# Performance work log

Hardware: AMD Instinct MI355X
Metric: run time of the kernel (lower is better)

Reference implementation:

```python
import jax, jax.numpy as jnp
import numpy as np

N = 100000   # nodes
E = 1600000  # edges (avg degree 16)
D = 128      # input feature dim
DIMS = [D, 64, 32, 16, 4]
K = 3


def setup_inputs() -> dict:
    key = jax.random.key(0)
    ks = jax.random.split(key, 8)
    inp = {
        "x": jax.random.normal(ks[0], (N, D), jnp.float32),
        "edge_index": jax.random.randint(ks[1], (2, E), 0, N, dtype=jnp.int32).astype(jnp.int64),
        "edge_weight": jax.random.uniform(ks[2], (E,), jnp.float32),
    }
    for i in range(4):
        fin, fout = DIMS[i], DIMS[i + 1]
        inp[f"W{i+1}"] = jax.random.normal(ks[3 + i], (K, fin, fout), jnp.float32) / np.sqrt(fin)
        inp[f"b{i+1}"] = jnp.zeros((fout,), jnp.float32)
    return inp


def reference(x, edge_index, edge_weight, W1, b1, W2, b2, W3, b3, W4, b4):
    # ChebConv, K=3, normalization='sym', lambda_max=2 (PyG defaults).
    # Scaled Laplacian L~ = 2L/lambda_max - I = -D^{-1/2} A D^{-1/2}
    n = x.shape[0]
    src, dst = edge_index[0], edge_index[1]
    deg = jax.ops.segment_sum(edge_weight, src, num_segments=n)
    dinv = jnp.where(deg > 0, jax.lax.rsqrt(deg), 0.0)
    norm = dinv[src] * edge_weight * dinv[dst]  # [E]

    def Lmul(h):  # L~ @ h  == -A_norm @ h
        return -jax.ops.segment_sum(norm[:, None] * h[src], dst, num_segments=n)

    def cheb(h, W, b):
        # Tx_0 = h, Tx_1 = L~ h, Tx_2 = 2 L~ Tx_1 - Tx_0
        Tx0 = h
        Tx1 = Lmul(h)
        Tx2 = 2.0 * Lmul(Tx1) - Tx0
        return Tx0 @ W[0] + Tx1 @ W[1] + Tx2 @ W[2] + b

    # training=False -> dropout is identity
    h = jax.nn.relu(cheb(x, W1, b1))
    h = jax.nn.relu(cheb(h, W2, b2))
    h = jax.nn.relu(cheb(h, W3, b3))
    h = cheb(h, W4, b4)
    return jax.nn.log_softmax(h, axis=1)
```

## Files before the change

### kernel.cpp

```cpp
#include <hip/hip_runtime.h>
#include <math.h>

#define D_IN 128
typedef unsigned short ushort_t;
typedef __attribute__((ext_vector_type(8))) short short8;
typedef __attribute__((ext_vector_type(4))) float f32x4;

__device__ __forceinline__ float bf2f(ushort_t u) {
    union { unsigned i; float f; } x;
    x.i = ((unsigned)u) << 16;
    return x.f;
}
__device__ __forceinline__ ushort_t f2bf(float f) {
    unsigned i = __float_as_uint(f);
    unsigned r = (i + 0x7fffu + ((i >> 16) & 1u)) >> 16;
    return (ushort_t)r;
}

#define CH 256
#define CHS 8
#define CAP 6144
#define MAXCH 512
#define NBIN 256

__global__ __launch_bounds__(256) void bin2_kernel(const int* __restrict__ src,
                                                   const int* __restrict__ dst,
                                                   const float* __restrict__ w,
                                                   int* __restrict__ gcA, int* __restrict__ gcB,
                                                   int2* __restrict__ stA,
                                                   int2* __restrict__ stB, int E, int nch) {
    __shared__ int cntA[MAXCH], baseA[MAXCH], posA[MAXCH];
    __shared__ int cntB[MAXCH], baseB[MAXCH], posB[MAXCH];
    for (int i = threadIdx.x; i < nch; i += 256) {
        cntA[i] = 0; posA[i] = 0; cntB[i] = 0; posB[i] = 0;
    }
    __syncthreads();
    int per = (E + gridDim.x - 1) / gridDim.x;
    int e0 = blockIdx.x * per, e1 = min(E, e0 + per);
    for (int e = e0 + threadIdx.x; e < e1; e += 256) {
        atomicAdd(&cntA[dst[e] >> CHS], 1);
        atomicAdd(&cntB[src[e] >> CHS], 1);
    }
    __syncthreads();
    for (int i = threadIdx.x; i < nch; i += 256) {
        int c = cntA[i];
        baseA[i] = c ? atomicAdd(&gcA[i], c) : 0;
        c = cntB[i];
        baseB[i] = c ? atomicAdd(&gcB[i], c) : 0;
    }
    __syncthreads();
    for (int e = e0 + threadIdx.x; e < e1; e += 256) {
        int s = src[e], d = dst[e];
        int wb = __float_as_int(w[e]);
        int cA = d >> CHS;
        int pA = baseA[cA] + atomicAdd(&posA[cA], 1);
        if (pA < CAP) {
            int2 o;
            o.x = s | ((d & (CH - 1)) << 17);
            o.y = wb;
            stA[(size_t)cA * CAP + pA] = o;
        }
        int cB = s >> CHS;
        int pB = baseB[cB] + atomicAdd(&posB[cB], 1);
        if (pB < CAP) {
            int2 o;
            o.x = s & (CH - 1);
            o.y = wb;
            stB[(size_t)cB * CAP + pB] = o;
        }
    }
}

__global__ __launch_bounds__(256) void deg_chunk_kernel(const int* __restrict__ gcB,
                                                        const int2* __restrict__ stB,
                                                        float* __restrict__ deg, int n) {
    __shared__ float acc[CH];
    int c = blockIdx.x, kb = blockIdx.y, KB = gridDim.y;
    for (int i = threadIdx.x; i < CH; i += 256) acc[i] = 0.f;
    __syncthreads();
    int m = min(gcB[c], CAP);
    int per = (m + KB - 1) / KB;
    int i0 = kb * per, i1 = min(m, i0 + per);
    size_t base = (size_t)c * CAP;
    for (int i = i0 + threadIdx.x; i < i1; i += 256) {
        int2 v = stB[base + i];
        atomicAdd(&acc[v.x], __int_as_float(v.y));
    }
    __syncthreads();
    int nb = c * CH, lim = min(CH, n - nb);
    for (int i = threadIdx.x; i < lim; i += 256) {
        float v = acc[i];
        if (v != 0.f) atomicAdd(&deg[nb + i], v);
    }
}

__global__ void dinv_kernel(float* __restrict__ deg, int n) {
    int i = blockIdx.x * blockDim.x + threadIdx.x;
    if (i >= n) return;
    float d = deg[i];
    deg[i] = (d > 0.f) ? rsqrtf(d) : 0.f;
}

__global__ __launch_bounds__(512) void cbase_kernel(const int* __restrict__ gcA,
                                                    int* __restrict__ cbase,
                                                    int* __restrict__ rp, int nch, int n) {
    __shared__ int sd[MAXCH];
    int t = threadIdx.x;
    sd[t] = (t < nch) ? min(gcA[t], CAP) : 0;
    __syncthreads();
    for (int off = 1; off < MAXCH; off <<= 1) {
        int y = (t >= off) ? sd[t - off] : 0;
        __syncthreads();
        sd[t] += y;
        __syncthreads();
    }
    if (t < nch) cbase[t] = (t > 0) ? sd[t - 1] : 0;
    if (t == 0) rp[n] = sd[nch - 1];
}

__global__ __launch_bounds__(256) void csr_chunk_kernel(const int* __restrict__ gcA,
                                                        const int* __restrict__ cbase,
                                                        const int2* __restrict__ stA,
                                                        const float* __restrict__ dinv,
                                                        int* __restrict__ rp,
                                                        int2* __restrict__ cv, int n) {
    __shared__ int lcnt[CH];
    __shared__ int lrp[CH];
    __shared__ float ldinv[CH];
    __shared__ int sdata[256];
    int c = blockIdx.x;
    int nb = c * CH, lim = min(CH, n - nb);
    int m = min(gcA[c], CAP);
    size_t sb = (size_t)c * CAP;
    int t = threadIdx.x;
    if (t < CH) lcnt[t] = 0;
    if (t < lim) ldinv[t] = dinv[nb + t];
    __syncthreads();
    for (int i = t; i < m; i += 256) atomicAdd(&lcnt[stA[sb + i].x >> 17], 1);
    __syncthreads();
    int v = (t < CH) ? lcnt[t] : 0;
    sdata[t] = v;
    __syncthreads();
    for (int off = 1; off < 256; off <<= 1) {
        int y = (t >= off) ? sdata[t - off] : 0;
        __syncthreads();
        sdata[t] += y;
        __syncthreads();
    }
    if (t < CH) lrp[t] = sdata[t] - v;
    __syncthreads();
    int base = cbase[c];
    if (t < lim) rp[nb + t] = base + lrp[t];
    if (t < CH) lcnt[t] = 0;
    __syncthreads();
    for (int i = t; i < m; i += 256) {
        int2 sv = stA[sb + i];
        int sN = sv.x & 0x1FFFF;
        int dl = sv.x >> 17;
        float nv = dinv[sN] * __int_as_float(sv.y) * ldinv[dl];
        int o = base + lrp[dl] + atomicAdd(&lcnt[dl], 1);
        int2 oo;
        oo.x = sN;
        oo.y = __float_as_int(nv);
        cv[o] = oo;
    }
}

__global__ void wt_all_kernel(const float* __restrict__ W1, const float* __restrict__ W2,
                              const float* __restrict__ W3, ushort_t* __restrict__ Wt1,
                              ushort_t* __restrict__ Wt2, ushort_t* __restrict__ Wt3) {
    int i = blockIdx.x * blockDim.x + threadIdx.x;
    if (i < 24576) {
        int m = i / 8192, rem = i % 8192, f = rem / 64, g = rem % 64;
        Wt1[((size_t)(m * 64 + g)) * 128 + f] = f2bf(W1[i]);
    } else if (i < 24576 + 6144) {
        int j = i - 24576;
        int m = j / 2048, rem = j % 2048, f = rem / 32, g = rem % 32;
        Wt2[((size_t)(m * 32 + g)) * 64 + f] = f2bf(W2[j]);
    } else if (i < 24576 + 6144 + 1536) {
        int j = i - 24576 - 6144;
        int m = j / 512, rem = j % 512, f = rem / 16, g = rem % 16;
        Wt3[((size_t)(m * 16 + g)) * 32 + f] = f2bf(W3[j]);
    }
}

template <int F, int G, bool A_BF16>
__global__ __launch_bounds__(256) void gemm_mfma(const void* __restrict__ Hv,
                                                 const ushort_t* __restrict__ Wt,
                                                 ushort_t* __restrict__ YA16,
                                                 ushort_t* __restrict__ YB16,
                                                 ushort_t* __restrict__ C16, int n) {
    constexpr int CT = G / 16;
    const int tid = threadIdx.x;
    const int wave = tid >> 6;
    const int lane = tid & 63;
    const int l16 = lane & 15;
    const int lk8 = (lane >> 4) * 8;

    const int rowBase = blockIdx.x * 64 + wave * 16;
    int rA = rowBase + l16;
    if (rA >= n) rA = n - 1;

    f32x4 acc[3][CT];
#pragma unroll
    for (int m = 0; m < 3; ++m)
#pragma unroll
        for (int ct = 0; ct < CT; ++ct)
#pragma unroll
            for (int j = 0; j < 4; ++j) acc[m][ct][j] = 0.f;

#pragma unroll
    for (int ks = 0; ks < F; ks += 32) {
        short8 a;
        if constexpr (A_BF16) {
            a = *(const short8*)((const ushort_t*)Hv + (size_t)rA * F + ks + lk8);
        } else {
            const float* ap = (const float*)Hv + (size_t)rA * F + ks + lk8;
            float4 f0 = *(const float4*)ap;
            float4 f1 = *(const float4*)(ap + 4);
            a[0] = (short)f2bf(f0.x);
            a[1] = (short)f2bf(f0.y);
            a[2] = (short)f2bf(f0.z);
            a[3] = (short)f2bf(f0.w);
            a[4] = (short)f2bf(f1.x);
            a[5] = (short)f2bf(f1.y);
            a[6] = (short)f2bf(f1.z);
            a[7] = (short)f2bf(f1.w);
        }
#pragma unroll
        for (int m = 0; m < 3; ++m) {
#pragma unroll
            for (int ct = 0; ct < CT; ++ct) {
                short8 b = *(const short8*)(Wt + ((size_t)(m * G + ct * 16 + l16)) * F +
                                            ks + lk8);
                acc[m][ct] = __builtin_amdgcn_mfma_f32_16x16x32_bf16(a, b, acc[m][ct], 0, 0, 0);
            }
        }
    }

    const int r0 = rowBase + (lane >> 4) * 4;
#pragma unroll
    for (int ct = 0; ct < CT; ++ct) {
        const int col = ct * 16 + l16;
#pragma unroll
        for (int j = 0; j < 4; ++j) {
            int r = r0 + j;
            if (r < n) {
                size_t idx = (size_t)r * G + col;
                YA16[idx] = f2bf(acc[0][ct][j] - acc[2][ct][j]);
                YB16[idx] = f2bf(acc[1][ct][j]);
                C16[idx] = f2bf(acc[2][ct][j]);
            }
        }
    }
}

template <int G, int MODE>
__global__ __launch_bounds__(256) void spmm_bf16(const ushort_t* __restrict__ Hg,
                                                 const ushort_t* __restrict__ Yres,
                                                 const float* __restrict__ bias,
                                                 ushort_t* __restrict__ outS,
                                                 const int2* __restrict__ cv,
                                                 const int* __restrict__ rp, int n) {
    constexpr int TPR = G / 4;
    constexpr int RPB = 256 / TPR;
    int row = blockIdx.x * RPB + threadIdx.x / TPR;
    if (row >= n) return;
    int g = (threadIdx.x % TPR) * 4;
    float a0 = 0.f, a1 = 0.f, a2 = 0.f, a3 = 0.f;
    int e = rp[row], e1 = rp[row + 1];
    for (; e + 4 <= e1; e += 4) {
        int2 c0 = cv[e], c1 = cv[e + 1], c2 = cv[e + 2], c3 = cv[e + 3];
        ushort4 h0 = *(const ushort4*)(Hg + (size_t)c0.x * G + g);
        ushort4 h1 = *(const ushort4*)(Hg + (size_t)c1.x * G + g);
        ushort4 h2 = *(const ushort4*)(Hg + (size_t)c2.x * G + g);
        ushort4 h3 = *(const ushort4*)(Hg + (size_t)c3.x * G + g);
        float v0 = __int_as_float(c0.y), v1 = __int_as_float(c1.y);
        float v2 = __int_as_float(c2.y), v3 = __int_as_float(c3.y);
        a0 = fmaf(v0, bf2f(h0.x), a0); a1 = fmaf(v0, bf2f(h0.y), a1);
        a2 = fmaf(v0, bf2f(h0.z), a2); a3 = fmaf(v0, bf2f(h0.w), a3);
        a0 = fmaf(v1, bf2f(h1.x), a0); a1 = fmaf(v1, bf2f(h1.y), a1);
        a2 = fmaf(v1, bf2f(h1.z), a2); a3 = fmaf(v1, bf2f(h1.w), a3);
        a0 = fmaf(v2, bf2f(h2.x), a0); a1 = fmaf(v2, bf2f(h2.y), a1);
        a2 = fmaf(v2, bf2f(h2.z), a2); a3 = fmaf(v2, bf2f(h2.w), a3);
        a0 = fmaf(v3, bf2f(h3.x), a0); a1 = fmaf(v3, bf2f(h3.y), a1);
        a2 = fmaf(v3, bf2f(h3.z), a2); a3 = fmaf(v3, bf2f(h3.w), a3);
    }
    for (; e < e1; ++e) {
        int2 c = cv[e];
        float v = __int_as_float(c.y);
        ushort4 hv = *(const ushort4*)(Hg + (size_t)c.x * G + g);
        a0 = fmaf(v, bf2f(hv.x), a0);
        a1 = fmaf(v, bf2f(hv.y), a1);
        a2 = fmaf(v, bf2f(hv.z), a2);
        a3 = fmaf(v, bf2f(hv.w), a3);
    }
    size_t idx = (size_t)row * G + g;
    ushort4 yv = *(const ushort4*)(Yres + idx);
    ushort4 o;
    if (MODE == 1) {
        o.x = f2bf(bf2f(yv.x) - 2.f * a0);
        o.y = f2bf(bf2f(yv.y) - 2.f * a1);
        o.z = f2bf(bf2f(yv.z) - 2.f * a2);
        o.w = f2bf(bf2f(yv.w) - 2.f * a3);
    } else {
        float4 bv = *(const float4*)(bias + g);
        o.x = f2bf(fmaxf(bf2f(yv.x) - a0 + bv.x, 0.f));
        o.y = f2bf(fmaxf(bf2f(yv.y) - a1 + bv.y, 0.f));
        o.z = f2bf(fmaxf(bf2f(yv.z) - a2 + bv.z, 0.f));
        o.w = f2bf(fmaxf(bf2f(yv.w) - a3 + bv.w, 0.f));
    }
    *(ushort4*)(outS + idx) = o;
}


__global__ void gemm4(const ushort_t* __restrict__ H, const float* __restrict__ W,
                      float* __restrict__ YA, float* __restrict__ YB, float* __restrict__ C,
                      int n) {
    __shared__ float Ws[3 * 16 * 4];
    if (threadIdx.x < 192) Ws[threadIdx.x] = W[threadIdx.x];
    __syncthreads();
    int i = blockIdx.x * blockDim.x + threadIdx.x;
    if (i >= n) return;
    const ushort_t* h = H + (size_t)i * 16;
    float a[4], b[4], c[4];
#pragma unroll
    for (int g = 0; g < 4; ++g) a[g] = b[g] = c[g] = 0.f;
#pragma unroll
    for (int j = 0; j < 2; ++j) {
        short8 hv = *(const short8*)(h + j * 8);
#pragma unroll
        for (int k = 0; k < 8; ++k) {
            int f = j * 8 + k;
            float hf = bf2f((ushort_t)hv[k]);
#pragma unroll
            for (int g = 0; g < 4; ++g) {
                a[g] = fmaf(hf, Ws[f * 4 + g], a[g]);
                b[g] = fmaf(hf, Ws[64 + f * 4 + g], b[g]);
                c[g] = fmaf(hf, Ws[128 + f * 4 + g], c[g]);
            }
        }
    }
    float4 oa, ob, oc;
    oa.x = a[0] - c[0]; oa.y = a[1] - c[1]; oa.z = a[2] - c[2]; oa.w = a[3] - c[3];
    ob.x = b[0]; ob.y = b[1]; ob.z = b[2]; ob.w = b[3];
    oc.x = c[0]; oc.y = c[1]; oc.z = c[2]; oc.w = c[3];
    *(float4*)(YA + (size_t)i * 4) = oa;
    *(float4*)(YB + (size_t)i * 4) = ob;
    *(float4*)(C + (size_t)i * 4) = oc;
}

__global__ void spmm4(const float* __restrict__ C, const float* __restrict__ YB,
                      float* __restrict__ S, const int2* __restrict__ cv,
                      const int* __restrict__ rp, int n) {
    int row = blockIdx.x * blockDim.x + threadIdx.x;
    if (row >= n) return;
    float a0 = 0.f, a1 = 0.f, a2 = 0.f, a3 = 0.f;
    int e1 = rp[row + 1];
    for (int e = rp[row]; e < e1; ++e) {
        int2 c = cv[e];
        float v = __int_as_float(c.y);
        float4 cvv = *(const float4*)(C + (size_t)c.x * 4);
        a0 = fmaf(v, cvv.x, a0);
        a1 = fmaf(v, cvv.y, a1);
        a2 = fmaf(v, cvv.z, a2);
        a3 = fmaf(v, cvv.w, a3);
    }
    float4 yb = *(const float4*)(YB + (size_t)row * 4);
    float4 o;
    o.x = yb.x - 2.f * a0;
    o.y = yb.y - 2.f * a1;
    o.z = yb.z - 2.f * a2;
    o.w = yb.w - 2.f * a3;
    *(float4*)(S + (size_t)row * 4) = o;
}

__global__ void layer4_final(const float* __restrict__ S, const float* __restrict__ YA,
                             const float* __restrict__ b, float* __restrict__ out,
                             const int2* __restrict__ cv, const int* __restrict__ rp, int n) {
    int row = blockIdx.x * blockDim.x + threadIdx.x;
    if (row >= n) return;
    float a0 = 0.f, a1 = 0.f, a2 = 0.f, a3 = 0.f;
    int e1 = rp[row + 1];
    for (int e = rp[row]; e < e1; ++e) {
        int2 c = cv[e];
        float v = __int_as_float(c.y);
        float4 sv = *(const float4*)(S + (size_t)c.x * 4);
        a0 = fmaf(v, sv.x, a0);
        a1 = fmaf(v, sv.y, a1);
        a2 = fmaf(v, sv.z, a2);
        a3 = fmaf(v, sv.w, a3);
    }
    float4 ya = *(const float4*)(YA + (size_t)row * 4);
    float o0 = ya.x - a0 + b[0];
    float o1 = ya.y - a1 + b[1];
    float o2 = ya.z - a2 + b[2];
    float o3 = ya.w - a3 + b[3];
    float m = fmaxf(fmaxf(o0, o1), fmaxf(o2, o3));
    float s = expf(o0 - m) + expf(o1 - m) + expf(o2 - m) + expf(o3 - m);
    float ls = m + logf(s);
    float4 r;
    r.x = o0 - ls;
    r.y = o1 - ls;
    r.z = o2 - ls;
    r.w = o3 - ls;
    *(float4*)(out + (size_t)row * 4) = r;
}


static inline char* align_up(char* p, size_t a) {
    return (char*)(((uintptr_t)p + a - 1) & ~(uintptr_t)(a - 1));
}

extern "C" void kernel_launch(void* const* d_in, const int* in_sizes, int n_in,
                              void* d_out, int out_size, void* d_ws, size_t ws_size,
                              hipStream_t stream) {
    const float* x = (const float*)d_in[0];
    const int* ei = (const int*)d_in[1];
    const float* ew = (const float*)d_in[2];
    const float* W1 = (const float*)d_in[3];
    const float* b1 = (const float*)d_in[4];
    const float* W2 = (const float*)d_in[5];
    const float* b2 = (const float*)d_in[6];
    const float* W3 = (const float*)d_in[7];
    const float* b3 = (const float*)d_in[8];
    const float* W4 = (const float*)d_in[9];
    const float* b4 = (const float*)d_in[10];
    float* out = (float*)d_out;

    const int n = in_sizes[0] / D_IN;
    const int E = in_sizes[2];
    const int* src = ei;
    const int* dst = ei + E;
    const int nch = (n + CH - 1) / CH;

    char* p = (char*)d_ws;
    int2* cv = (int2*)p;          p += (size_t)E * 8;
    float* deg = (float*)p;       p += (size_t)n * 4;
    int* rp = (int*)p;            p = align_up(p + (size_t)(n + 1) * 4, 64);
    int* gcA = (int*)p;           p += MAXCH * 4;
    int* gcB = (int*)p;           p += MAXCH * 4;
    int* cbase = (int*)p;         p = align_up(p + MAXCH * 4, 64);
    ushort_t* Wt1 = (ushort_t*)p; p = align_up(p + (size_t)192 * 128 * 2, 64);
    ushort_t* Wt2 = (ushort_t*)p; p = align_up(p + (size_t)96 * 64 * 2, 64);
    ushort_t* Wt3 = (ushort_t*)p; p = align_up(p + (size_t)48 * 32 * 2, 64);
    char* big = p;
    ushort_t* YA16 = (ushort_t*)big;
    ushort_t* YB16 = (ushort_t*)(big + (size_t)n * 64 * 2);
    ushort_t* C16 = (ushort_t*)(big + (size_t)n * 64 * 2 * 2);
    ushort_t* S16 = (ushort_t*)(big + (size_t)n * 64 * 2 * 3);
    int2* stA = (int2*)big;
    int2* stB = (int2*)(big + (size_t)nch * CAP * 8);
    p = align_up(big + (size_t)n * 64 * 2 * 4, 64);
    ushort_t* H1 = (ushort_t*)p;  p = align_up(p + (size_t)n * 64 * 2, 64);
    ushort_t* H2 = (ushort_t*)p;  p = align_up(p + (size_t)n * 32 * 2, 64);
    ushort_t* H3 = (ushort_t*)p;  p = align_up(p + (size_t)n * 16 * 2, 64);
    float* YA4 = (float*)p;       p = align_up(p + (size_t)n * 4 * 4, 64);
    float* YB4 = (float*)p;       p = align_up(p + (size_t)n * 4 * 4, 64);
    float* C4 = (float*)p;        p = align_up(p + (size_t)n * 4 * 4, 64);
    float* S4 = (float*)p;        p = align_up(p + (size_t)n * 4 * 4, 64);

    const int TB = 256;
    int nb256 = (n + TB - 1) / TB;
    int gm = (n + 63) / 64;

    hipMemsetAsync(deg, 0, (size_t)n * 4, stream);
    hipMemsetAsync(gcA, 0, MAXCH * 4 * 2, stream);
    bin2_kernel<<<NBIN, 256, 0, stream>>>(src, dst, ew, gcA, gcB, stA, stB, E, nch);
    {
        dim3 dg(nch, 4);
        deg_chunk_kernel<<<dg, 256, 0, stream>>>(gcB, stB, deg, n);
    }
    dinv_kernel<<<nb256, TB, 0, stream>>>(deg, n);
    cbase_kernel<<<1, MAXCH, 0, stream>>>(gcA, cbase, rp, nch, n);
    csr_chunk_kernel<<<nch, 256, 0, stream>>>(gcA, cbase, stA, deg, rp, cv, n);

    wt_all_kernel<<<(24576 + 6144 + 1536 + 255) / 256, 256, 0, stream>>>(W1, W2, W3, Wt1,
                                                                         Wt2, Wt3);

    {
        constexpr int G = 64;
        gemm_mfma<128, G, false><<<gm, 256, 0, stream>>>(x, Wt1, YA16, YB16, C16, n);
        int sb = (n + (1024 / G) - 1) / (1024 / G);
        spmm_bf16<G, 1><<<sb, 256, 0, stream>>>(C16, YB16, nullptr, S16, cv, rp, n);
        spmm_bf16<G, 2><<<sb, 256, 0, stream>>>(S16, YA16, b1, H1, cv, rp, n);
    }
    {
        constexpr int G = 32;
        gemm_mfma<64, G, true><<<gm, 256, 0, stream>>>(H1, Wt2, YA16, YB16, C16, n);
        int sb = (n + (1024 / G) - 1) / (1024 / G);
        spmm_bf16<G, 1><<<sb, 256, 0, stream>>>(C16, YB16, nullptr, S16, cv, rp, n);
        spmm_bf16<G, 2><<<sb, 256, 0, stream>>>(S16, YA16, b2, H2, cv, rp, n);
    }
    {
        constexpr int G = 16;
        gemm_mfma<32, G, true><<<gm, 256, 0, stream>>>(H2, Wt3, YA16, YB16, C16, n);
        int sb = (n + (1024 / G) - 1) / (1024 / G);
        spmm_bf16<G, 1><<<sb, 256, 0, stream>>>(C16, YB16, nullptr, S16, cv, rp, n);
        spmm_bf16<G, 2><<<sb, 256, 0, stream>>>(S16, YA16, b3, H3, cv, rp, n);
    }
    {
        gemm4<<<nb256, 256, 0, stream>>>(H3, W4, YA4, YB4, C4, n);
        spmm4<<<nb256, 256, 0, stream>>>(C4, YB4, S4, cv, rp, n);
        layer4_final<<<nb256, 256, 0, stream>>>(S4, YA4, b4, out, cv, rp, n);
    }
}
```

Measured before the change: 399.7 us.

## Widen binning blocks, double GEMM row tile per wave, unroll SpMM gather by 8

Three separate changes. The edge-binning kernel now launches 1024-thread blocks instead of 256, giving more parallelism per block while keeping the same shared-memory histograms. The MFMA GEMM has each wave compute two 16-row tiles, so every weight fragment load feeds two MFMAs, at the cost of more accumulator registers. The SpMM gather loop adds an 8-way unrolled stage that issues eight index and feature loads before the FMAs, to keep more memory requests in flight, which also raises register pressure.

```diff
diff --git a/kernel.cpp b/kernel.cpp
--- a/kernel.cpp
+++ b/kernel.cpp
@@ -23,33 +23,34 @@
 #define MAXCH 512
 #define NBIN 256
 
-__global__ __launch_bounds__(256) void bin2_kernel(const int* __restrict__ src,
-                                                   const int* __restrict__ dst,
-                                                   const float* __restrict__ w,
-                                                   int* __restrict__ gcA, int* __restrict__ gcB,
-                                                   int2* __restrict__ stA,
-                                                   int2* __restrict__ stB, int E, int nch) {
+__global__ __launch_bounds__(1024) void bin2_kernel(const int* __restrict__ src,
+                                                    const int* __restrict__ dst,
+                                                    const float* __restrict__ w,
+                                                    int* __restrict__ gcA, int* __restrict__ gcB,
+                                                    int2* __restrict__ stA,
+                                                    int2* __restrict__ stB, int E, int nch) {
     __shared__ int cntA[MAXCH], baseA[MAXCH], posA[MAXCH];
     __shared__ int cntB[MAXCH], baseB[MAXCH], posB[MAXCH];
-    for (int i = threadIdx.x; i < nch; i += 256) {
+    const int NT = 1024;
+    for (int i = threadIdx.x; i < nch; i += NT) {
         cntA[i] = 0; posA[i] = 0; cntB[i] = 0; posB[i] = 0;
     }
     __syncthreads();
     int per = (E + gridDim.x - 1) / gridDim.x;
     int e0 = blockIdx.x * per, e1 = min(E, e0 + per);
-    for (int e = e0 + threadIdx.x; e < e1; e += 256) {
+    for (int e = e0 + threadIdx.x; e < e1; e += NT) {
         atomicAdd(&cntA[dst[e] >> CHS], 1);
         atomicAdd(&cntB[src[e] >> CHS], 1);
     }
     __syncthreads();
-    for (int i = threadIdx.x; i < nch; i += 256) {
+    for (int i = threadIdx.x; i < nch; i += NT) {
         int c = cntA[i];
         baseA[i] = c ? atomicAdd(&gcA[i], c) : 0;
         c = cntB[i];
         baseB[i] = c ? atomicAdd(&gcB[i], c) : 0;
     }
     __syncthreads();
-    for (int e = e0 + threadIdx.x; e < e1; e += 256) {
+    for (int e = e0 + threadIdx.x; e < e1; e += NT) {
         int s = src[e], d = dst[e];
         int wb = __float_as_int(w[e]);
         int cA = d >> CHS;
@@ -197,35 +198,43 @@
     const int l16 = lane & 15;
     const int lk8 = (lane >> 4) * 8;
 
-    const int rowBase = blockIdx.x * 64 + wave * 16;
-    int rA = rowBase + l16;
-    if (rA >= n) rA = n - 1;
-
-    f32x4 acc[3][CT];
-#pragma unroll
-    for (int m = 0; m < 3; ++m)
-#pragma unroll
-        for (int ct = 0; ct < CT; ++ct)
-#pragma unroll
-            for (int j = 0; j < 4; ++j) acc[m][ct][j] = 0.f;
+    const int rowBase = blockIdx.x * 128 + wave * 32;
+    int rA0 = rowBase + l16;
+    int rA1 = rowBase + 16 + l16;
+    if (rA0 >= n) rA0 = n - 1;
+    if (rA1 >= n) rA1 = n - 1;
+
+    f32x4 acc[2][3][CT];
+#pragma unroll
+    for (int h = 0; h < 2; ++h)
+#pragma unroll
+        for (int m = 0; m < 3; ++m)
+#pragma unroll
+            for (int ct = 0; ct < CT; ++ct)
+#pragma unroll
+                for (int j = 0; j < 4; ++j) acc[h][m][ct][j] = 0.f;
 
 #pragma unroll
     for (int ks = 0; ks < F; ks += 32) {
-        short8 a;
+        short8 a0, a1;
         if constexpr (A_BF16) {
-            a = *(const short8*)((const ushort_t*)Hv + (size_t)rA * F + ks + lk8);
+            a0 = *(const short8*)((const ushort_t*)Hv + (size_t)rA0 * F + ks + lk8);
+            a1 = *(const short8*)((const ushort_t*)Hv + (size_t)rA1 * F + ks + lk8);
         } else {
-            const float* ap = (const float*)Hv + (size_t)rA * F + ks + lk8;
-            float4 f0 = *(const float4*)ap;
-            float4 f1 = *(const float4*)(ap + 4);
-            a[0] = (short)f2bf(f0.x);
-            a[1] = (short)f2bf(f0.y);
-            a[2] = (short)f2bf(f0.z);
-            a[3] = (short)f2bf(f0.w);
-            a[4] = (short)f2bf(f1.x);
-            a[5] = (short)f2bf(f1.y);
-            a[6] = (short)f2bf(f1.z);
-            a[7] = (short)f2bf(f1.w);
+            const float* ap0 = (const float*)Hv + (size_t)rA0 * F + ks + lk8;
+            const float* ap1 = (const float*)Hv + (size_t)rA1 * F + ks + lk8;
+            float4 f00 = *(const float4*)ap0;
+            float4 f01 = *(const float4*)(ap0 + 4);
+            float4 f10 = *(const float4*)ap1;
+            float4 f11 = *(const float4*)(ap1 + 4);
+            a0[0] = (short)f2bf(f00.x); a0[1] = (short)f2bf(f00.y);
+            a0[2] = (short)f2bf(f00.z); a0[3] = (short)f2bf(f00.w);
+            a0[4] = (short)f2bf(f01.x); a0[5] = (short)f2bf(f01.y);
+            a0[6] = (short)f2bf(f01.z); a0[7] = (short)f2bf(f01.w);
+            a1[0] = (short)f2bf(f10.x); a1[1] = (short)f2bf(f10.y);
+            a1[2] = (short)f2bf(f10.z); a1[3] = (short)f2bf(f10.w);
+            a1[4] = (short)f2bf(f11.x); a1[5] = (short)f2bf(f11.y);
+            a1[6] = (short)f2bf(f11.z); a1[7] = (short)f2bf(f11.w);
         }
 #pragma unroll
         for (int m = 0; m < 3; ++m) {
@@ -233,23 +242,27 @@
             for (int ct = 0; ct < CT; ++ct) {
                 short8 b = *(const short8*)(Wt + ((size_t)(m * G + ct * 16 + l16)) * F +
                                             ks + lk8);
-                acc[m][ct] = __builtin_amdgcn_mfma_f32_16x16x32_bf16(a, b, acc[m][ct], 0, 0, 0);
+                acc[0][m][ct] = __builtin_amdgcn_mfma_f32_16x16x32_bf16(a0, b, acc[0][m][ct], 0, 0, 0);
+                acc[1][m][ct] = __builtin_amdgcn_mfma_f32_16x16x32_bf16(a1, b, acc[1][m][ct], 0, 0, 0);
             }
         }
     }
 
-    const int r0 = rowBase + (lane >> 4) * 4;
-#pragma unroll
-    for (int ct = 0; ct < CT; ++ct) {
-        const int col = ct * 16 + l16;
-#pragma unroll
-        for (int j = 0; j < 4; ++j) {
-            int r = r0 + j;
-            if (r < n) {
-                size_t idx = (size_t)r * G + col;
-                YA16[idx] = f2bf(acc[0][ct][j] - acc[2][ct][j]);
-                YB16[idx] = f2bf(acc[1][ct][j]);
-                C16[idx] = f2bf(acc[2][ct][j]);
+#pragma unroll
+    for (int h = 0; h < 2; ++h) {
+        const int r0 = rowBase + h * 16 + (lane >> 4) * 4;
+#pragma unroll
+        for (int ct = 0; ct < CT; ++ct) {
+            const int col = ct * 16 + l16;
+#pragma unroll
+            for (int j = 0; j < 4; ++j) {
+                int r = r0 + j;
+                if (r < n) {
+                    size_t idx = (size_t)r * G + col;
+                    YA16[idx] = f2bf(acc[h][0][ct][j] - acc[h][2][ct][j]);
+                    YB16[idx] = f2bf(acc[h][1][ct][j]);
+                    C16[idx] = f2bf(acc[h][2][ct][j]);
+                }
             }
         }
     }
@@ -269,22 +282,37 @@
     int g = (threadIdx.x % TPR) * 4;
     float a0 = 0.f, a1 = 0.f, a2 = 0.f, a3 = 0.f;
     int e = rp[row], e1 = rp[row + 1];
+    for (; e + 8 <= e1; e += 8) {
+        int2 c[8];
+        ushort4 h[8];
+#pragma unroll
+        for (int k = 0; k < 8; ++k) c[k] = cv[e + k];
+#pragma unroll
+        for (int k = 0; k < 8; ++k) h[k] = *(const ushort4*)(Hg + (size_t)c[k].x * G + g);
+#pragma unroll
+        for (int k = 0; k < 8; ++k) {
+            float v = __int_as_float(c[k].y);
+            a0 = fmaf(v, bf2f(h[k].x), a0);
+            a1 = fmaf(v, bf2f(h[k].y), a1);
+            a2 = fmaf(v, bf2f(h[k].z), a2);
+            a3 = fmaf(v, bf2f(h[k].w), a3);
+        }
+    }
     for (; e + 4 <= e1; e += 4) {
-        int2 c0 = cv[e], c1 = cv[e + 1], c2 = cv[e + 2], c3 = cv[e + 3];
-        ushort4 h0 = *(const ushort4*)(Hg + (size_t)c0.x * G + g);
-        ushort4 h1 = *(const ushort4*)(Hg + (size_t)c1.x * G + g);
-        ushort4 h2 = *(const ushort4*)(Hg + (size_t)c2.x * G + g);
-        ushort4 h3 = *(const ushort4*)(Hg + (size_t)c3.x * G + g);
-        float v0 = __int_as_float(c0.y), v1 = __int_as_float(c1.y);
-        float v2 = __int_as_float(c2.y), v3 = __int_as_float(c3.y);
-        a0 = fmaf(v0, bf2f(h0.x), a0); a1 = fmaf(v0, bf2f(h0.y), a1);
-        a2 = fmaf(v0, bf2f(h0.z), a2); a3 = fmaf(v0, bf2f(h0.w), a3);
-        a0 = fmaf(v1, bf2f(h1.x), a0); a1 = fmaf(v1, bf2f(h1.y), a1);
-        a2 = fmaf(v1, bf2f(h1.z), a2); a3 = fmaf(v1, bf2f(h1.w), a3);
-        a0 = fmaf(v2, bf2f(h2.x), a0); a1 = fmaf(v2, bf2f(h2.y), a1);
-        a2 = fmaf(v2, bf2f(h2.z), a2); a3 = fmaf(v2, bf2f(h2.w), a3);
-        a0 = fmaf(v3, bf2f(h3.x), a0); a1 = fmaf(v3, bf2f(h3.y), a1);
-        a2 = fmaf(v3, bf2f(h3.z), a2); a3 = fmaf(v3, bf2f(h3.w), a3);
+        int2 c[4];
+        ushort4 h[4];
+#pragma unroll
+        for (int k = 0; k < 4; ++k) c[k] = cv[e + k];
+#pragma unroll
+        for (int k = 0; k < 4; ++k) h[k] = *(const ushort4*)(Hg + (size_t)c[k].x * G + g);
+#pragma unroll
+        for (int k = 0; k < 4; ++k) {
+            float v = __int_as_float(c[k].y);
+            a0 = fmaf(v, bf2f(h[k].x), a0);
+            a1 = fmaf(v, bf2f(h[k].y), a1);
+            a2 = fmaf(v, bf2f(h[k].z), a2);
+            a3 = fmaf(v, bf2f(h[k].w), a3);
+        }
     }
     for (; e < e1; ++e) {
         int2 c = cv[e];
@@ -462,11 +490,11 @@
 
     const int TB = 256;
     int nb256 = (n + TB - 1) / TB;
-    int gm = (n + 63) / 64;
+    int gm = (n + 127) / 128;
 
     hipMemsetAsync(deg, 0, (size_t)n * 4, stream);
     hipMemsetAsync(gcA, 0, MAXCH * 4 * 2, stream);
-    bin2_kernel<<<NBIN, 256, 0, stream>>>(src, dst, ew, gcA, gcB, stA, stB, E, nch);
+    bin2_kernel<<<NBIN, 1024, 0, stream>>>(src, dst, ew, gcA, gcB, stA, stB, E, nch);
     {
         dim3 dg(nch, 4);
         deg_chunk_kernel<<<dg, 256, 0, stream>>>(gcB, stB, deg, n);
```

After: 369.9 us. 7.5% less time.
